# Kernel optimization log

Hardware: AMD Instinct MI355X
Metric: run time of the kernel (lower is better)

## Reference

```python
import jax, jax.numpy as jnp
import numpy as np

M, K, N, GROUP = 64, 4096, 11008, 128
NGROUPS = K // GROUP  # 32


def setup_inputs() -> dict:
    key = jax.random.key(0)
    k1, k2, k3, k4, k5 = jax.random.split(key, 5)
    x = jax.random.normal(k1, (M, K), dtype=jnp.float32)
    # packed int4 weights: 8 nibbles per int32, full 32-bit entropy
    qweight = jax.random.bits(k2, (K // 8, N), dtype=jnp.uint32).astype(jnp.int32)
    qzeros = jax.random.bits(k3, (NGROUPS, N // 8), dtype=jnp.uint32).astype(jnp.int32)
    scales = jax.random.uniform(k4, (NGROUPS, N), dtype=jnp.float32, minval=0.001, maxval=0.02)
    bias = jax.random.normal(k5, (N,), dtype=jnp.float32) * 0.01
    return {"x": x, "qweight": qweight, "qzeros": qzeros, "scales": scales, "bias": bias}


def dequantize(qweight, qzeros, scales):
    shifts = jnp.arange(8, dtype=jnp.int32) * 4  # nibble bit offsets 0..28
    # unpack weights: [K//8, N] -> [K//8, 8, N] -> [NGROUPS, GROUP, N]
    w = (jnp.right_shift(qweight[:, None, :], shifts[None, :, None]) & 15)
    w = w.reshape(-1, GROUP, qweight.shape[1])
    # unpack zeros: [NGROUPS, N//8] -> [NGROUPS, N//8, 8] -> [NGROUPS, 1, N]; GPTQ stores zero-1
    z = (jnp.right_shift(qzeros[:, :, None], shifts[None, None, :]) & 15) + 1
    z = z.reshape(z.shape[0], 1, -1)
    # scale * (q - zero), per group: [NGROUPS, GROUP, N] -> [K, N]
    W = scales[:, None, :] * (w - z).astype(scales.dtype)
    return W.reshape(-1, W.shape[2])


def reference(x, qweight, qzeros, scales, bias):
    W = dequantize(qweight, qzeros, scales)  # [K, N] fp32
    return jnp.matmul(x, W.astype(x.dtype)) + bias
```

## Files before the change

kernel.cpp:

```cpp
#include <hip/hip_runtime.h>
#include <hip/hip_bf16.h>

namespace {

constexpr int MM = 64;
constexpr int KK = 4096;
constexpr int NN = 11008;
constexpr int NZROW = NN / 8;
constexpr int BN = 128;
constexpr int KSPLIT = 8;
constexpr int KSEG = KK / KSPLIT;
constexpr int NTILES = NN / BN;
constexpr int BK = 32;
constexpr int RS = 20;

typedef float f32x4 __attribute__((ext_vector_type(4)));
typedef short s16x8 __attribute__((ext_vector_type(8)));
typedef int   i32x4 __attribute__((ext_vector_type(4)));

__device__ __forceinline__ int pack_bf16(float a, float b) {
  union { __hip_bfloat162 h; int i; } u;
  u.h.x = __float2bfloat16(a);
  u.h.y = __float2bfloat16(b);
  return u.i;
}

__global__ __launch_bounds__(256) void prep_kernel(
    const float* __restrict__ bias, float* __restrict__ out)
{
  const int i = blockIdx.x * 256 + threadIdx.x;
  out[i] = bias[i % NN];
}

__global__ __launch_bounds__(256, 2) void gptq_gemm_kernel(
    const float* __restrict__ x, const int* __restrict__ qw,
    const int* __restrict__ qz, const float* __restrict__ scales,
    float* __restrict__ out)
{
  __shared__ int As[MM * RS];
  __shared__ int Bs[BN * RS];

  const int tid  = threadIdx.x;
  const int wave = tid >> 6;
  const int lane = tid & 63;
  const int c    = lane & 15;
  const int quad = lane >> 4;

  const int ntile  = blockIdx.x % NTILES;
  const int ks     = blockIdx.x / NTILES;
  const int n0     = ntile * BN;
  const int kbase0 = ks * KSEG;

  const int am   = tid >> 2;
  const int aseg = tid & 3;
  const int bu0  = tid >> 7;
  const int bn   = tid & 127;
  const int mrow = wave * 16 + quad * 4;

  f32x4 acc[8];
  #pragma unroll
  for (int t = 0; t < 8; ++t) acc[t] = {0.f, 0.f, 0.f, 0.f};

  for (int chunk = 0; chunk < KSEG / BK; ++chunk) {
    const int kc = kbase0 + chunk * BK;

    const float* xp = x + am * KK + kc + aseg * 8;
    f32x4 f0 = *(const f32x4*)xp;
    f32x4 f1 = *(const f32x4*)(xp + 4);
    i32x4 pa;
    pa.x = pack_bf16(f0.x, f0.y);
    pa.y = pack_bf16(f0.z, f0.w);
    pa.z = pack_bf16(f1.x, f1.y);
    pa.w = pack_bf16(f1.z, f1.w);
    *(i32x4*)&As[am * RS + aseg * 4] = pa;

    const int g = kc >> 7;
    const int N = n0 + bn;
    const float s  = scales[g * NN + N];
    const int  zn  = (qz[g * NZROW + (N >> 3)] >> ((N & 7) * 4)) & 15;
    const float C  = (float)(0x800000 + zn + 1);
    const int r0 = kc >> 3;
    #pragma unroll
    for (int h = 0; h < 2; ++h) {
      const int u = bu0 + 2 * h;
      const int v = qw[(r0 + u) * NN + N];
      float w0 = s * (__int_as_float(((v      ) & 15) | 0x4B000000) - C);
      float w1 = s * (__int_as_float(((v >>  4) & 15) | 0x4B000000) - C);
      float w2 = s * (__int_as_float(((v >>  8) & 15) | 0x4B000000) - C);
      float w3 = s * (__int_as_float(((v >> 12) & 15) | 0x4B000000) - C);
      float w4 = s * (__int_as_float(((v >> 16) & 15) | 0x4B000000) - C);
      float w5 = s * (__int_as_float(((v >> 20) & 15) | 0x4B000000) - C);
      float w6 = s * (__int_as_float(((v >> 24) & 15) | 0x4B000000) - C);
      float w7 = s * (__int_as_float(((v >> 28) & 15) | 0x4B000000) - C);
      i32x4 pb;
      pb.x = pack_bf16(w0, w1);
      pb.y = pack_bf16(w2, w3);
      pb.z = pack_bf16(w4, w5);
      pb.w = pack_bf16(w6, w7);
      *(i32x4*)&Bs[bn * RS + u * 4] = pb;
    }

    __syncthreads();

    const s16x8 af = *(const s16x8*)&As[(wave * 16 + c) * RS + quad * 4];
    #pragma unroll
    for (int t = 0; t < 8; ++t) {
      const s16x8 bfr = *(const s16x8*)&Bs[(t * 16 + c) * RS + quad * 4];
      acc[t] = __builtin_amdgcn_mfma_f32_16x16x32_bf16(af, bfr, acc[t], 0, 0, 0);
    }

    __syncthreads();
  }

  #pragma unroll
  for (int t = 0; t < 8; ++t) {
    const int N = n0 + t * 16 + c;
    atomicAdd(&out[(mrow + 0) * NN + N], acc[t].x);
    atomicAdd(&out[(mrow + 1) * NN + N], acc[t].y);
    atomicAdd(&out[(mrow + 2) * NN + N], acc[t].z);
    atomicAdd(&out[(mrow + 3) * NN + N], acc[t].w);
  }
}

}

extern "C" void kernel_launch(void* const* d_in, const int* in_sizes, int n_in,
                              void* d_out, int out_size, void* d_ws, size_t ws_size,
                              hipStream_t stream) {
  const float* x      = (const float*)d_in[0];
  const int*   qw     = (const int*)d_in[1];
  const int*   qz     = (const int*)d_in[2];
  const float* scales = (const float*)d_in[3];
  const float* bias   = (const float*)d_in[4];
  float* out = (float*)d_out;

  prep_kernel<<<(MM * NN) / 256, 256, 0, stream>>>(bias, out);
  gptq_gemm_kernel<<<NTILES * KSPLIT, 256, 0, stream>>>(x, qw, qz, scales, out);
}
```

Measured before the change: 116.1 us.

## Double-buffer LDS with register prefetch and replace atomics with workspace split-K reduce

The main loop now double-buffers shared memory and prefetches the next chunk's x, qweight, scales and zeros into registers, so one barrier per chunk replaces two. Each thread now dequantizes two adjacent columns with vectorized loads, and the grid index is remapped so the split-K blocks of one N tile are launched next to each other. When the workspace is large enough, partial sums go to a per-split workspace with plain stores and a separate reduce kernel adds them with the bias, in place of atomics. The cost is more registers, which may hurt occupancy, plus extra workspace traffic of about 22 MB written and read.

```diff
diff --git a/kernel.cpp b/kernel.cpp
--- a/kernel.cpp
+++ b/kernel.cpp
@@ -12,11 +12,17 @@
 constexpr int KSEG = KK / KSPLIT;
 constexpr int NTILES = NN / BN;
 constexpr int BK = 32;
+constexpr int NCH = KSEG / BK;
 constexpr int RS = 20;
+constexpr int ABUF = MM * RS;
+constexpr int BBUF = BN * RS;
+constexpr size_t WS_NEED = (size_t)KSPLIT * MM * NN * 4;
 
 typedef float f32x4 __attribute__((ext_vector_type(4)));
+typedef float f32x2 __attribute__((ext_vector_type(2)));
 typedef short s16x8 __attribute__((ext_vector_type(8)));
 typedef int   i32x4 __attribute__((ext_vector_type(4)));
+typedef int   i32x2 __attribute__((ext_vector_type(2)));
 
 __device__ __forceinline__ int pack_bf16(float a, float b) {
   union { __hip_bfloat162 h; int i; } u;
@@ -32,13 +38,26 @@
   out[i] = bias[i % NN];
 }
 
+__global__ __launch_bounds__(256) void reduce_kernel(
+    const float* __restrict__ ws, const float* __restrict__ bias,
+    float* __restrict__ out)
+{
+  const int i4 = (blockIdx.x * 256 + threadIdx.x) * 4;
+  f32x4 acc = *(const f32x4*)(bias + (i4 % NN));
+  #pragma unroll
+  for (int s = 0; s < KSPLIT; ++s)
+    acc += *(const f32x4*)(ws + (size_t)s * (MM * NN) + i4);
+  *(f32x4*)(out + i4) = acc;
+}
+
+template<bool ATOMIC>
 __global__ __launch_bounds__(256, 2) void gptq_gemm_kernel(
     const float* __restrict__ x, const int* __restrict__ qw,
     const int* __restrict__ qz, const float* __restrict__ scales,
     float* __restrict__ out)
 {
-  __shared__ int As[MM * RS];
-  __shared__ int Bs[BN * RS];
+  __shared__ int As[2 * ABUF];
+  __shared__ int Bs[2 * BBUF];
 
   const int tid  = threadIdx.x;
   const int wave = tid >> 6;
@@ -46,79 +65,112 @@
   const int c    = lane & 15;
   const int quad = lane >> 4;
 
-  const int ntile  = blockIdx.x % NTILES;
-  const int ks     = blockIdx.x / NTILES;
+  const int ks     = blockIdx.x & 7;
+  const int ntile  = blockIdx.x >> 3;
   const int n0     = ntile * BN;
   const int kbase0 = ks * KSEG;
 
   const int am   = tid >> 2;
   const int aseg = tid & 3;
-  const int bu0  = tid >> 7;
-  const int bn   = tid & 127;
+  const int bu   = tid & 3;
+  const int cp   = tid >> 2;
+  const int Ncp  = n0 + 2 * cp;
   const int mrow = wave * 16 + quad * 4;
+
+  const float* xrow = x + am * KK + aseg * 8;
 
   f32x4 acc[8];
   #pragma unroll
   for (int t = 0; t < 8; ++t) acc[t] = {0.f, 0.f, 0.f, 0.f};
 
-  for (int chunk = 0; chunk < KSEG / BK; ++chunk) {
-    const int kc = kbase0 + chunk * BK;
+  f32x4 pA0[2], pA1[2];
+  i32x2 pB[2];
+  f32x2 pS[2];
+  int   pZ[2];
 
-    const float* xp = x + am * KK + kc + aseg * 8;
-    f32x4 f0 = *(const f32x4*)xp;
-    f32x4 f1 = *(const f32x4*)(xp + 4);
+  auto pf = [&](int i, int sl) {
+    const int kc = kbase0 + i * BK;
+    pA0[sl] = *(const f32x4*)(xrow + kc);
+    pA1[sl] = *(const f32x4*)(xrow + kc + 4);
+    const int g  = kc >> 7;
+    const int r0 = kc >> 3;
+    pB[sl] = *(const i32x2*)(qw + (size_t)(r0 + bu) * NN + Ncp);
+    pS[sl] = *(const f32x2*)(scales + g * NN + Ncp);
+    pZ[sl] = qz[g * NZROW + (Ncp >> 3)];
+  };
+
+  pf(0, 0);
+
+  #pragma unroll
+  for (int i = 0; i < NCH; ++i) {
+    const int sl = i & 1;
+    if (i + 1 < NCH) pf(i + 1, sl ^ 1);
+
+    int* Abuf = As + sl * ABUF;
     i32x4 pa;
-    pa.x = pack_bf16(f0.x, f0.y);
-    pa.y = pack_bf16(f0.z, f0.w);
-    pa.z = pack_bf16(f1.x, f1.y);
-    pa.w = pack_bf16(f1.z, f1.w);
-    *(i32x4*)&As[am * RS + aseg * 4] = pa;
+    pa.x = pack_bf16(pA0[sl].x, pA0[sl].y);
+    pa.y = pack_bf16(pA0[sl].z, pA0[sl].w);
+    pa.z = pack_bf16(pA1[sl].x, pA1[sl].y);
+    pa.w = pack_bf16(pA1[sl].z, pA1[sl].w);
+    *(i32x4*)&Abuf[am * RS + aseg * 4] = pa;
 
-    const int g = kc >> 7;
-    const int N = n0 + bn;
-    const float s  = scales[g * NN + N];
-    const int  zn  = (qz[g * NZROW + (N >> 3)] >> ((N & 7) * 4)) & 15;
-    const float C  = (float)(0x800000 + zn + 1);
-    const int r0 = kc >> 3;
-    #pragma unroll
-    for (int h = 0; h < 2; ++h) {
-      const int u = bu0 + 2 * h;
-      const int v = qw[(r0 + u) * NN + N];
-      float w0 = s * (__int_as_float(((v      ) & 15) | 0x4B000000) - C);
-      float w1 = s * (__int_as_float(((v >>  4) & 15) | 0x4B000000) - C);
-      float w2 = s * (__int_as_float(((v >>  8) & 15) | 0x4B000000) - C);
-      float w3 = s * (__int_as_float(((v >> 12) & 15) | 0x4B000000) - C);
-      float w4 = s * (__int_as_float(((v >> 16) & 15) | 0x4B000000) - C);
-      float w5 = s * (__int_as_float(((v >> 20) & 15) | 0x4B000000) - C);
-      float w6 = s * (__int_as_float(((v >> 24) & 15) | 0x4B000000) - C);
-      float w7 = s * (__int_as_float(((v >> 28) & 15) | 0x4B000000) - C);
-      i32x4 pb;
-      pb.x = pack_bf16(w0, w1);
-      pb.y = pack_bf16(w2, w3);
-      pb.z = pack_bf16(w4, w5);
-      pb.w = pack_bf16(w6, w7);
-      *(i32x4*)&Bs[bn * RS + u * 4] = pb;
-    }
+    int* Bbuf = Bs + sl * BBUF;
+    const float s0 = pS[sl].x, s1 = pS[sl].y;
+    const int sh0 = (Ncp & 7) * 4;
+    const int z0  = (pZ[sl] >> sh0) & 15;
+    const int z1  = (pZ[sl] >> (sh0 + 4)) & 15;
+    const float C0 = (float)(0x800000 + z0 + 1);
+    const float C1 = (float)(0x800000 + z1 + 1);
+    const int v0 = pB[sl].x, v1 = pB[sl].y;
+    i32x4 pb0, pb1;
+    pb0.x = pack_bf16(s0 * (__int_as_float(((v0      ) & 15) | 0x4B000000) - C0),
+                      s0 * (__int_as_float(((v0 >>  4) & 15) | 0x4B000000) - C0));
+    pb0.y = pack_bf16(s0 * (__int_as_float(((v0 >>  8) & 15) | 0x4B000000) - C0),
+                      s0 * (__int_as_float(((v0 >> 12) & 15) | 0x4B000000) - C0));
+    pb0.z = pack_bf16(s0 * (__int_as_float(((v0 >> 16) & 15) | 0x4B000000) - C0),
+                      s0 * (__int_as_float(((v0 >> 20) & 15) | 0x4B000000) - C0));
+    pb0.w = pack_bf16(s0 * (__int_as_float(((v0 >> 24) & 15) | 0x4B000000) - C0),
+                      s0 * (__int_as_float(((v0 >> 28) & 15) | 0x4B000000) - C0));
+    pb1.x = pack_bf16(s1 * (__int_as_float(((v1      ) & 15) | 0x4B000000) - C1),
+                      s1 * (__int_as_float(((v1 >>  4) & 15) | 0x4B000000) - C1));
+    pb1.y = pack_bf16(s1 * (__int_as_float(((v1 >>  8) & 15) | 0x4B000000) - C1),
+                      s1 * (__int_as_float(((v1 >> 12) & 15) | 0x4B000000) - C1));
+    pb1.z = pack_bf16(s1 * (__int_as_float(((v1 >> 16) & 15) | 0x4B000000) - C1),
+                      s1 * (__int_as_float(((v1 >> 20) & 15) | 0x4B000000) - C1));
+    pb1.w = pack_bf16(s1 * (__int_as_float(((v1 >> 24) & 15) | 0x4B000000) - C1),
+                      s1 * (__int_as_float(((v1 >> 28) & 15) | 0x4B000000) - C1));
+    *(i32x4*)&Bbuf[(2 * cp    ) * RS + bu * 4] = pb0;
+    *(i32x4*)&Bbuf[(2 * cp + 1) * RS + bu * 4] = pb1;
 
-    __syncthreads();
+    __asm__ volatile("s_waitcnt lgkmcnt(0)\n\ts_barrier" ::: "memory");
 
-    const s16x8 af = *(const s16x8*)&As[(wave * 16 + c) * RS + quad * 4];
+    const s16x8 af = *(const s16x8*)&Abuf[(wave * 16 + c) * RS + quad * 4];
     #pragma unroll
     for (int t = 0; t < 8; ++t) {
-      const s16x8 bfr = *(const s16x8*)&Bs[(t * 16 + c) * RS + quad * 4];
+      const s16x8 bfr = *(const s16x8*)&Bbuf[(t * 16 + c) * RS + quad * 4];
       acc[t] = __builtin_amdgcn_mfma_f32_16x16x32_bf16(af, bfr, acc[t], 0, 0, 0);
     }
-
-    __syncthreads();
   }
 
-  #pragma unroll
-  for (int t = 0; t < 8; ++t) {
-    const int N = n0 + t * 16 + c;
-    atomicAdd(&out[(mrow + 0) * NN + N], acc[t].x);
-    atomicAdd(&out[(mrow + 1) * NN + N], acc[t].y);
-    atomicAdd(&out[(mrow + 2) * NN + N], acc[t].z);
-    atomicAdd(&out[(mrow + 3) * NN + N], acc[t].w);
+  if (ATOMIC) {
+    #pragma unroll
+    for (int t = 0; t < 8; ++t) {
+      const int N = n0 + t * 16 + c;
+      atomicAdd(&out[(mrow + 0) * NN + N], acc[t].x);
+      atomicAdd(&out[(mrow + 1) * NN + N], acc[t].y);
+      atomicAdd(&out[(mrow + 2) * NN + N], acc[t].z);
+      atomicAdd(&out[(mrow + 3) * NN + N], acc[t].w);
+    }
+  } else {
+    float* wsp = out + (size_t)ks * (MM * NN);
+    #pragma unroll
+    for (int t = 0; t < 8; ++t) {
+      const int N = n0 + t * 16 + c;
+      wsp[(mrow + 0) * NN + N] = acc[t].x;
+      wsp[(mrow + 1) * NN + N] = acc[t].y;
+      wsp[(mrow + 2) * NN + N] = acc[t].z;
+      wsp[(mrow + 3) * NN + N] = acc[t].w;
+    }
   }
 }
 
@@ -134,6 +186,12 @@
   const float* bias   = (const float*)d_in[4];
   float* out = (float*)d_out;
 
-  prep_kernel<<<(MM * NN) / 256, 256, 0, stream>>>(bias, out);
-  gptq_gemm_kernel<<<NTILES * KSPLIT, 256, 0, stream>>>(x, qw, qz, scales, out);
+  if (ws_size >= WS_NEED) {
+    float* ws = (float*)d_ws;
+    gptq_gemm_kernel<false><<<NTILES * KSPLIT, 256, 0, stream>>>(x, qw, qz, scales, ws);
+    reduce_kernel<<<(MM * NN) / 1024, 256, 0, stream>>>(ws, bias, out);
+  } else {
+    prep_kernel<<<(MM * NN) / 256, 256, 0, stream>>>(bias, out);
+    gptq_gemm_kernel<true><<<NTILES * KSPLIT, 256, 0, stream>>>(x, qw, qz, scales, out);
+  }
 }
```

Result: faster. 97.22 us (-16.3%).
